# Kernel tuning notes

Hardware: AMD Instinct MI355X
Metric: run time of the kernel (lower is better)

The kernel has to match this reference:

```python
import jax, jax.numpy as jnp
import numpy as np

N, S, D = 8, 2048, 2048   # batch, seq, input_size
O = 2048                  # output_size
E = 8                     # num experts
K = 2                     # top_k


def setup_inputs() -> dict:
    key = jax.random.key(0)
    ks = jax.random.split(key, 5)
    scale_in = 1.0 / np.sqrt(D)
    x = jax.random.normal(ks[0], (N, S, D), dtype=jnp.float32)
    gate_w = jax.random.uniform(ks[1], (D, E), dtype=jnp.float32, minval=-scale_in, maxval=scale_in)
    gate_b = jax.random.uniform(ks[2], (E,), dtype=jnp.float32, minval=-scale_in, maxval=scale_in)
    expert_w = jax.random.uniform(ks[3], (E, D, O), dtype=jnp.float32, minval=-scale_in, maxval=scale_in)
    expert_b = jax.random.uniform(ks[4], (E, O), dtype=jnp.float32, minval=-scale_in, maxval=scale_in)
    return {"x": x, "gate_w": gate_w, "gate_b": gate_b,
            "expert_w": expert_w, "expert_b": expert_b}


def reference(x, gate_w, gate_b, expert_w, expert_b):
    # gate logits [N,S,E] and top-k expert indices per token
    gate_logits = jnp.einsum('nsd,de->nse', x, gate_w) + gate_b
    _, top_idx = jax.lax.top_k(gate_logits, K)               # [N,S,K]
    # dense all-expert Linear+ReLU: [N,S,E,O]
    all_out = jax.nn.relu(jnp.einsum('nsd,edo->nseo', x, expert_w) + expert_b)
    # gather the top_k experts' outputs per token -> [N,S,K,O]
    sel = jnp.take_along_axis(all_out, top_idx[..., None], axis=2)
    # original averages expert outputs (gate values unused in mixing)
    return sel.mean(axis=2)                                   # [N,S,O]
```

## Files before the change

kernel.cpp:

```cpp
#include <hip/hip_runtime.h>
#include <stdint.h>

#define NS_TOK 16384
#define DIM 2048
#define OUTD 2048
#define NEXP 8
#define NPAIR 28

typedef __attribute__((ext_vector_type(8))) short short8;
typedef __attribute__((ext_vector_type(4))) float f32x4;
typedef __attribute__((address_space(3))) uint32_t lds_u32;
typedef __attribute__((address_space(1))) const uint32_t gbl_u32;

__device__ __forceinline__ unsigned short f2bf(float f) {
  union { float f; uint32_t u; } v; v.f = f;
  uint32_t r = v.u + 0x7fffu + ((v.u >> 16) & 1u);
  return (unsigned short)(r >> 16);
}

__device__ __forceinline__ void gld_lds16(const void* g, void* l) {
  __builtin_amdgcn_global_load_lds((gbl_u32*)g, (lds_u32*)l, 16, 0, 0);
}

__constant__ int cPE1[NPAIR] = {0,0,0,0,0,0,0, 1,1,1,1,1,1, 2,2,2,2,2, 3,3,3,3, 4,4,4, 5,5, 6};
__constant__ int cPE2[NPAIR] = {1,2,3,4,5,6,7, 2,3,4,5,6,7, 3,4,5,6,7, 4,5,6,7, 5,6,7, 6,7, 7};

__global__ void zero_counts(int* counts) {
  if (threadIdx.x < NPAIR) counts[threadIdx.x] = 0;
}

__global__ __launch_bounds__(256) void gate_topk(
    const float* __restrict__ x, const float* __restrict__ gw,
    const float* __restrict__ gb, unsigned short* __restrict__ xbf,
    int* __restrict__ counts, int* __restrict__ lists) {
  __shared__ float gwT[8 * 2048];
  const int t = threadIdx.x;
  const float4* gw4 = (const float4*)gw;
#pragma unroll
  for (int j = 0; j < 16; ++j) {
    const int i4 = j * 256 + t;
    const float4 v = gw4[i4];
    const int d = i4 >> 1;
    const int eh = (i4 & 1) * 4;
    gwT[(eh + 0) * 2048 + d] = v.x;
    gwT[(eh + 1) * 2048 + d] = v.y;
    gwT[(eh + 2) * 2048 + d] = v.z;
    gwT[(eh + 3) * 2048 + d] = v.w;
  }
  __syncthreads();

  const int wave = t >> 6;
  const int lane = t & 63;
  for (int p = 0; p < 4; ++p) {
    const int tok0 = blockIdx.x * 32 + wave * 8 + p * 2;
    const float* xr0 = x + (size_t)tok0 * DIM;
    unsigned short* xb0 = xbf + (size_t)tok0 * DIM;
    float a0[8] = {0.f, 0.f, 0.f, 0.f, 0.f, 0.f, 0.f, 0.f};
    float a1[8] = {0.f, 0.f, 0.f, 0.f, 0.f, 0.f, 0.f, 0.f};
#pragma unroll
    for (int it = 0; it < 8; ++it) {
      const int d0 = it * 256 + lane * 4;
      const float4 x0 = *(const float4*)(xr0 + d0);
      const float4 x1 = *(const float4*)(xr0 + DIM + d0);
      ushort4 p0, p1;
      p0.x = f2bf(x0.x); p0.y = f2bf(x0.y); p0.z = f2bf(x0.z); p0.w = f2bf(x0.w);
      p1.x = f2bf(x1.x); p1.y = f2bf(x1.y); p1.z = f2bf(x1.z); p1.w = f2bf(x1.w);
      *(ushort4*)(xb0 + d0) = p0;
      *(ushort4*)(xb0 + DIM + d0) = p1;
#pragma unroll
      for (int e = 0; e < 8; ++e) {
        const float4 g = *(const float4*)(&gwT[e * 2048 + d0]);
        a0[e] += x0.x * g.x + x0.y * g.y + x0.z * g.z + x0.w * g.w;
        a1[e] += x1.x * g.x + x1.y * g.y + x1.z * g.z + x1.w * g.w;
      }
    }
#pragma unroll
    for (int e = 0; e < 8; ++e) {
#pragma unroll
      for (int off = 32; off > 0; off >>= 1) {
        a0[e] += __shfl_xor(a0[e], off);
        a1[e] += __shfl_xor(a1[e], off);
      }
    }
    if (lane < 2) {
      const float* aa = (lane == 0) ? a0 : a1;
      const int tok = tok0 + lane;
      float bv = -3.4e38f, sv = -3.4e38f;
      int bi = 0, si = 0;
#pragma unroll
      for (int ee = 0; ee < 8; ++ee) {
        const float v = aa[ee] + gb[ee];
        if (v > bv) { sv = bv; si = bi; bv = v; bi = ee; }
        else if (v > sv) { sv = v; si = ee; }
      }
      const int e1 = (bi < si) ? bi : si;
      const int e2 = (bi < si) ? si : bi;
      const int pi = 7 * e1 - (e1 * (e1 - 1)) / 2 + (e2 - e1 - 1);
      const int pos = atomicAdd(&counts[pi], 1);
      lists[(size_t)pi * NS_TOK + pos] = tok;
    }
  }
}

__global__ __launch_bounds__(256) void wconv(const float* __restrict__ w,
                                             unsigned short* __restrict__ wt) {
  __shared__ unsigned short s[64 * 66];
  const int e = blockIdx.z;
  const int d0 = blockIdx.y * 64;
  const int o0 = blockIdx.x * 64;
  const int t = threadIdx.x;
  const float* wp = w + (size_t)e * DIM * OUTD + (size_t)d0 * OUTD + o0;
#pragma unroll
  for (int p = 0; p < 4; ++p) {
    const int lin = p * 1024 + t * 4;
    const int dl = lin >> 6;
    const int ol = lin & 63;
    const float4 v = *(const float4*)(wp + (size_t)dl * OUTD + ol);
    uint32_t* sp = (uint32_t*)&s[dl * 66 + ol];
    sp[0] = (uint32_t)f2bf(v.x) | ((uint32_t)f2bf(v.y) << 16);
    sp[1] = (uint32_t)f2bf(v.z) | ((uint32_t)f2bf(v.w) << 16);
  }
  __syncthreads();
  unsigned short* wtp = wt + (size_t)e * OUTD * DIM + (size_t)o0 * DIM + d0;
#pragma unroll
  for (int p = 0; p < 2; ++p) {
    const int idx8 = p * 256 + t;
    const int ol2 = idx8 >> 3;
    const int dl2 = (idx8 & 7) * 8;
    ushort4 a, b;
    a.x = s[(dl2 + 0) * 66 + ol2]; a.y = s[(dl2 + 1) * 66 + ol2];
    a.z = s[(dl2 + 2) * 66 + ol2]; a.w = s[(dl2 + 3) * 66 + ol2];
    b.x = s[(dl2 + 4) * 66 + ol2]; b.y = s[(dl2 + 5) * 66 + ol2];
    b.z = s[(dl2 + 6) * 66 + ol2]; b.w = s[(dl2 + 7) * 66 + ol2];
    ushort4* op = (ushort4*)(wtp + (size_t)ol2 * DIM + dl2);
    op[0] = a; op[1] = b;
  }
}

__global__ __launch_bounds__(256, 2) void moe_gemm_pair(
    const unsigned short* __restrict__ xbf, const unsigned short* __restrict__ wt,
    const float* __restrict__ eb, const int* __restrict__ counts,
    const int* __restrict__ lists, float* __restrict__ out) {
  const int p = blockIdx.z;
  const int cnt = counts[p];
  const int r0 = blockIdx.y * 128;
  if (r0 >= cnt) return;
  const int e1 = cPE1[p];
  const int e2 = cPE2[p];

  __shared__ unsigned short sA[128 * 64];
  __shared__ unsigned short sB1[128 * 64];
  __shared__ unsigned short sB2[128 * 64];
  __shared__ int s_tok[128];

  const int tid = threadIdx.x;
  const int lane = tid & 63;
  const int w = tid >> 6;

  const int* lp = lists + (size_t)p * NS_TOK + r0;
  if (tid < 128) s_tok[tid] = (r0 + tid < cnt) ? lp[tid] : lp[0];
  __syncthreads();

  const unsigned short* agp[4];
  const unsigned short* b1gp[4];
  const size_t eoff = (size_t)(e2 - e1) * OUTD * DIM;
  const int gsub = tid & 7;
#pragma unroll
  for (int rd = 0; rd < 4; ++rd) {
    const int row = rd * 32 + (tid >> 3);
    const int gp = gsub ^ (row & 7);
    agp[rd] = xbf + (size_t)s_tok[row] * DIM + gp * 8;
    const int ncol = blockIdx.x * 128 + row;
    b1gp[rd] = wt + (size_t)e1 * OUTD * DIM + (size_t)ncol * DIM + gp * 8;
  }

  const int wrow = (w & 1) * 64;
  const int wcol = (w >> 1) * 64;
  const int kq = lane >> 4;
  const int l7 = lane & 7;
  const int ko[2] = {(kq ^ l7) * 16, ((4 + kq) ^ l7) * 16};
  int arow[4], brow[4];
#pragma unroll
  for (int i = 0; i < 4; ++i) {
    arow[i] = (wrow + i * 16 + (lane & 15)) * 128;
    brow[i] = (wcol + i * 16 + (lane & 15)) * 128;
  }

  f32x4 acc1[4][4] = {};
  f32x4 acc2[4][4] = {};
  char* sAc = (char*)sA;
  char* sB1c = (char*)sB1;
  char* sB2c = (char*)sB2;

  for (int kt = 0; kt < DIM / 64; ++kt) {
#pragma unroll
    for (int rd = 0; rd < 4; ++rd) {
      gld_lds16(agp[rd], sAc + (rd * 256 + w * 64) * 16);
      gld_lds16(b1gp[rd], sB1c + (rd * 256 + w * 64) * 16);
      gld_lds16(b1gp[rd] + eoff, sB2c + (rd * 256 + w * 64) * 16);
      agp[rd] += 64;
      b1gp[rd] += 64;
    }
    __syncthreads();
#pragma unroll
    for (int c = 0; c < 2; ++c) {
      short8 av[4], bv[4];
#pragma unroll
      for (int i = 0; i < 4; ++i) av[i] = *(const short8*)(sAc + arow[i] + ko[c]);
#pragma unroll
      for (int i = 0; i < 4; ++i) bv[i] = *(const short8*)(sB1c + brow[i] + ko[c]);
      __builtin_amdgcn_s_setprio(1);
#pragma unroll
      for (int mi = 0; mi < 4; ++mi)
#pragma unroll
        for (int ni = 0; ni < 4; ++ni)
          acc1[mi][ni] = __builtin_amdgcn_mfma_f32_16x16x32_bf16(
              av[mi], bv[ni], acc1[mi][ni], 0, 0, 0);
      __builtin_amdgcn_s_setprio(0);
#pragma unroll
      for (int i = 0; i < 4; ++i) bv[i] = *(const short8*)(sB2c + brow[i] + ko[c]);
      __builtin_amdgcn_s_setprio(1);
#pragma unroll
      for (int mi = 0; mi < 4; ++mi)
#pragma unroll
        for (int ni = 0; ni < 4; ++ni)
          acc2[mi][ni] = __builtin_amdgcn_mfma_f32_16x16x32_bf16(
              av[mi], bv[ni], acc2[mi][ni], 0, 0, 0);
      __builtin_amdgcn_s_setprio(0);
    }
    __syncthreads();
  }

  const int colb = blockIdx.x * 128 + wcol + (lane & 15);
  float bia1[4], bia2[4];
#pragma unroll
  for (int ni = 0; ni < 4; ++ni) {
    bia1[ni] = eb[e1 * OUTD + colb + ni * 16];
    bia2[ni] = eb[e2 * OUTD + colb + ni * 16];
  }
#pragma unroll
  for (int mi = 0; mi < 4; ++mi) {
#pragma unroll
    for (int r = 0; r < 4; ++r) {
      const int rl = wrow + mi * 16 + (lane >> 4) * 4 + r;
      if (r0 + rl < cnt) {
        float* orow = out + (size_t)s_tok[rl] * OUTD;
#pragma unroll
        for (int ni = 0; ni < 4; ++ni) {
          const float v1 = fmaxf(acc1[mi][ni][r] + bia1[ni], 0.0f);
          const float v2 = fmaxf(acc2[mi][ni][r] + bia2[ni], 0.0f);
          orow[colb + ni * 16] = 0.5f * (v1 + v2);
        }
      }
    }
  }
}

extern "C" void kernel_launch(void* const* d_in, const int* in_sizes, int n_in,
                              void* d_out, int out_size, void* d_ws, size_t ws_size,
                              hipStream_t stream) {
  const float* x  = (const float*)d_in[0];
  const float* gw = (const float*)d_in[1];
  const float* gb = (const float*)d_in[2];
  const float* ew = (const float*)d_in[3];
  const float* eb = (const float*)d_in[4];
  float* out = (float*)d_out;

  char* ws = (char*)d_ws;
  unsigned short* xbf = (unsigned short*)(ws);
  unsigned short* wt  = (unsigned short*)(ws + 67108864);
  int* counts         = (int*)(ws + 134217728);
  int* lists          = (int*)(ws + 134217984);

  zero_counts<<<1, 64, 0, stream>>>(counts);
  gate_topk<<<NS_TOK / 32, 256, 0, stream>>>(x, gw, gb, xbf, counts, lists);
  wconv<<<dim3(OUTD / 64, DIM / 64, NEXP), 256, 0, stream>>>(ew, wt);
  moe_gemm_pair<<<dim3(OUTD / 128, NS_TOK / 128, NPAIR), 256, 0, stream>>>(
      xbf, wt, eb, counts, lists, out);
}
```

Measured before the change: 741.5 us.

## Double-buffer LDS tiles with BK=32 to overlap global loads with MFMA

Shrinks the K-tile from 64 to 32 and allocates two LDS buffers for each of A, B1 and B2. The loads for tile k+1 are issued before computing on tile k, with one barrier per iteration instead of two, so memory latency can hide behind MFMA work. The swizzle and row-stride indexing are changed to match the narrower tile. LDS use stays the same, but the loop runs twice as many iterations with less work per barrier, so per-iteration overhead rises. There is also a risk that the compiler inserts vmcnt waits that serialize the async LDS loads anyway.

Measured after the change: 800.4 us. 7.9% more time.

```diff
diff --git a/kernel.cpp b/kernel.cpp
--- a/kernel.cpp
+++ b/kernel.cpp
@@ -6,6 +6,8 @@
 #define OUTD 2048
 #define NEXP 8
 #define NPAIR 28
+#define BK 32
+#define KT (DIM / BK)
 
 typedef __attribute__((ext_vector_type(8))) short short8;
 typedef __attribute__((ext_vector_type(4))) float f32x4;
@@ -148,9 +150,9 @@
   const int e1 = cPE1[p];
   const int e2 = cPE2[p];
 
-  __shared__ unsigned short sA[128 * 64];
-  __shared__ unsigned short sB1[128 * 64];
-  __shared__ unsigned short sB2[128 * 64];
+  __shared__ unsigned short sA[2 * 128 * BK];
+  __shared__ unsigned short sB1[2 * 128 * BK];
+  __shared__ unsigned short sB2[2 * 128 * BK];
   __shared__ int s_tok[128];
 
   const int tid = threadIdx.x;
@@ -161,75 +163,84 @@
   if (tid < 128) s_tok[tid] = (r0 + tid < cnt) ? lp[tid] : lp[0];
   __syncthreads();
 
-  const unsigned short* agp[4];
-  const unsigned short* b1gp[4];
+  const unsigned short* agp[2];
+  const unsigned short* b1gp[2];
   const size_t eoff = (size_t)(e2 - e1) * OUTD * DIM;
-  const int gsub = tid & 7;
-#pragma unroll
-  for (int rd = 0; rd < 4; ++rd) {
-    const int row = rd * 32 + (tid >> 3);
-    const int gp = gsub ^ (row & 7);
+#pragma unroll
+  for (int rd = 0; rd < 2; ++rd) {
+    const int row = rd * 64 + (tid >> 2);
+    const int gp = (tid & 3) ^ (row & 3);
     agp[rd] = xbf + (size_t)s_tok[row] * DIM + gp * 8;
     const int ncol = blockIdx.x * 128 + row;
     b1gp[rd] = wt + (size_t)e1 * OUTD * DIM + (size_t)ncol * DIM + gp * 8;
   }
 
-  const int wrow = (w & 1) * 64;
-  const int wcol = (w >> 1) * 64;
-  const int kq = lane >> 4;
-  const int l7 = lane & 7;
-  const int ko[2] = {(kq ^ l7) * 16, ((4 + kq) ^ l7) * 16};
-  int arow[4], brow[4];
-#pragma unroll
-  for (int i = 0; i < 4; ++i) {
-    arow[i] = (wrow + i * 16 + (lane & 15)) * 128;
-    brow[i] = (wcol + i * 16 + (lane & 15)) * 128;
-  }
-
-  f32x4 acc1[4][4] = {};
-  f32x4 acc2[4][4] = {};
   char* sAc = (char*)sA;
   char* sB1c = (char*)sB1;
   char* sB2c = (char*)sB2;
 
-  for (int kt = 0; kt < DIM / 64; ++kt) {
-#pragma unroll
-    for (int rd = 0; rd < 4; ++rd) {
-      gld_lds16(agp[rd], sAc + (rd * 256 + w * 64) * 16);
-      gld_lds16(b1gp[rd], sB1c + (rd * 256 + w * 64) * 16);
-      gld_lds16(b1gp[rd] + eoff, sB2c + (rd * 256 + w * 64) * 16);
-      agp[rd] += 64;
-      b1gp[rd] += 64;
-    }
+#define STAGE(b)                                                      \
+  do {                                                                \
+    char* dA = sAc + (b)*8192;                                        \
+    char* dB1 = sB1c + (b)*8192;                                      \
+    char* dB2 = sB2c + (b)*8192;                                      \
+    _Pragma("unroll")                                                 \
+    for (int rd = 0; rd < 2; ++rd) {                                  \
+      gld_lds16(agp[rd], dA + rd * 4096 + tid * 16);                  \
+      gld_lds16(b1gp[rd], dB1 + rd * 4096 + tid * 16);                \
+      gld_lds16(b1gp[rd] + eoff, dB2 + rd * 4096 + tid * 16);         \
+      agp[rd] += BK;                                                  \
+      b1gp[rd] += BK;                                                 \
+    }                                                                 \
+  } while (0)
+
+  const int wrow = (w & 1) * 64;
+  const int wcol = (w >> 1) * 64;
+  const int ko = (((lane >> 4) ^ (lane & 3)) * 16);
+  int arow[4], brow[4];
+#pragma unroll
+  for (int i = 0; i < 4; ++i) {
+    arow[i] = (wrow + i * 16 + (lane & 15)) * 64;
+    brow[i] = (wcol + i * 16 + (lane & 15)) * 64;
+  }
+
+  f32x4 acc1[4][4] = {};
+  f32x4 acc2[4][4] = {};
+
+  STAGE(0);
+  __syncthreads();
+
+  int cur = 0;
+  for (int kt = 0; kt < KT; ++kt) {
+    if (kt + 1 < KT) STAGE(cur ^ 1);
+    const char* pa = sAc + cur * 8192;
+    const char* pb1 = sB1c + cur * 8192;
+    const char* pb2 = sB2c + cur * 8192;
+    short8 av[4], b1v[4], b2v[4];
+#pragma unroll
+    for (int i = 0; i < 4; ++i) av[i] = *(const short8*)(pa + arow[i] + ko);
+#pragma unroll
+    for (int i = 0; i < 4; ++i) b1v[i] = *(const short8*)(pb1 + brow[i] + ko);
+#pragma unroll
+    for (int i = 0; i < 4; ++i) b2v[i] = *(const short8*)(pb2 + brow[i] + ko);
+    __builtin_amdgcn_s_setprio(1);
+#pragma unroll
+    for (int mi = 0; mi < 4; ++mi)
+#pragma unroll
+      for (int ni = 0; ni < 4; ++ni)
+        acc1[mi][ni] = __builtin_amdgcn_mfma_f32_16x16x32_bf16(
+            av[mi], b1v[ni], acc1[mi][ni], 0, 0, 0);
+#pragma unroll
+    for (int mi = 0; mi < 4; ++mi)
+#pragma unroll
+      for (int ni = 0; ni < 4; ++ni)
+        acc2[mi][ni] = __builtin_amdgcn_mfma_f32_16x16x32_bf16(
+            av[mi], b2v[ni], acc2[mi][ni], 0, 0, 0);
+    __builtin_amdgcn_s_setprio(0);
     __syncthreads();
-#pragma unroll
-    for (int c = 0; c < 2; ++c) {
-      short8 av[4], bv[4];
-#pragma unroll
-      for (int i = 0; i < 4; ++i) av[i] = *(const short8*)(sAc + arow[i] + ko[c]);
-#pragma unroll
-      for (int i = 0; i < 4; ++i) bv[i] = *(const short8*)(sB1c + brow[i] + ko[c]);
-      __builtin_amdgcn_s_setprio(1);
-#pragma unroll
-      for (int mi = 0; mi < 4; ++mi)
-#pragma unroll
-        for (int ni = 0; ni < 4; ++ni)
-          acc1[mi][ni] = __builtin_amdgcn_mfma_f32_16x16x32_bf16(
-              av[mi], bv[ni], acc1[mi][ni], 0, 0, 0);
-      __builtin_amdgcn_s_setprio(0);
-#pragma unroll
-      for (int i = 0; i < 4; ++i) bv[i] = *(const short8*)(sB2c + brow[i] + ko[c]);
-      __builtin_amdgcn_s_setprio(1);
-#pragma unroll
-      for (int mi = 0; mi < 4; ++mi)
-#pragma unroll
-        for (int ni = 0; ni < 4; ++ni)
-          acc2[mi][ni] = __builtin_amdgcn_mfma_f32_16x16x32_bf16(
-              av[mi], bv[ni], acc2[mi][ni], 0, 0, 0);
-      __builtin_amdgcn_s_setprio(0);
-    }
-    __syncthreads();
-  }
+    cur ^= 1;
+  }
+#undef STAGE
 
   const int colb = blockIdx.x * 128 + wcol + (lane & 15);
   float bia1[4], bia2[4];
```
